# Kernel optimization log

Hardware: AMD Instinct MI355X
Metric: run time of the kernel (lower is better)

Reference implementation:

```python
import jax, jax.numpy as jnp
import numpy as np

B, T, E, H, D = 4, 2048, 1024, 16, 64


def setup_inputs() -> dict:
    key = jax.random.key(0)
    k1, k2, k3, k4 = jax.random.split(key, 4)
    s = 1.0 / np.sqrt(E)
    return {
        "x": jax.random.normal(k1, (B, T, E), dtype=jnp.float32),
        "wj_w": jax.random.uniform(k2, (E, E), jnp.float32, -s, s),   # torch Linear weight (out,in)
        "wjv_w": jax.random.uniform(k3, (E, E), jnp.float32, -s, s),
        "wo_w": jax.random.uniform(k4, (E, H * D), jnp.float32, -s, s),
    }


def reference(x, wj_w, wjv_w, wo_w):
    b, t, e = x.shape
    # echo = x @ wj_w.T ; eb = echo @ wj_w  (F.linear with transposed weight)
    eb = (x @ wj_w.T) @ wj_w
    sc = jnp.sum(x * eb, axis=-1) / jnp.sqrt(jnp.asarray(e, x.dtype))  # (B,T)
    # rank-1 outer-product scores with strict-upper causal mask
    ja = sc[:, :, None] * sc[:, None, :]                               # (B,T,T)
    causal = jnp.tril(jnp.ones((t, t), dtype=bool))
    ja = jnp.where(causal[None], ja, -jnp.inf)
    ja = jax.nn.softmax(ja, axis=-1)                                   # (B,T,T)
    # values per head; attention map shared across heads (broadcast, not materialized)
    val = (x @ wjv_w.T).reshape(b, t, H, D)                            # (B,T,H,D)
    out = jnp.einsum("bts,bshd->bthd", ja, val)                       # (B,T,H,D)
    return out.reshape(b, t, H * D) @ wo_w.T                           # (B,T,E)
```

## Files before the change

### kernel.cpp

```cpp
#include <hip/hip_runtime.h>
#include <math.h>

#define R_ROWS 8192
#define T_SEQ  2048
#define E_DIM  1024
#define KC     32
#define KCR    256
#define PBATCH_ELEMS ((size_t)4352 * 512)

typedef __attribute__((ext_vector_type(8))) short short8;
typedef __attribute__((ext_vector_type(4))) float f32x4;

__device__ __forceinline__ ushort f2bf(float f) {
  uint u = __float_as_uint(f);
  u += 0x7FFFu + ((u >> 16) & 1u);
  return (ushort)(u >> 16);
}
__device__ __forceinline__ float bf2f(ushort h) {
  return __uint_as_float(((uint)h) << 16);
}


__device__ __forceinline__ void split_frag_unit(
    const float* __restrict__ in, ushort* __restrict__ hi,
    ushort* __restrict__ lo, int g)
{
  const int l = g & 15, h = (g >> 4) & 3;
  const int pq = g >> 6;
  const int q = pq & (KC - 1), p = pq >> 5;
  const size_t src = (size_t)(p * 16 + l) * 1024 + q * 32 + h * 8;
  const float4 v0 = *(const float4*)&in[src];
  const float4 v1 = *(const float4*)&in[src + 4];
  ushort hh[8], ll[8];
  const float v[8] = {v0.x, v0.y, v0.z, v0.w, v1.x, v1.y, v1.z, v1.w};
#pragma unroll
  for (int e = 0; e < 8; ++e) {
    hh[e] = f2bf(v[e]);
    ll[e] = f2bf(v[e] - bf2f(hh[e]));
  }
  *(uint4*)&hi[(size_t)g * 8] = *(const uint4*)hh;
  *(uint4*)&lo[(size_t)g * 8] = *(const uint4*)ll;
}

__device__ __forceinline__ void splitT_frag_unit(
    const float* __restrict__ in, ushort* __restrict__ hi,
    ushort* __restrict__ lo, int g)
{
  const int l = g & 15, h = (g >> 4) & 3;
  const int pq = g >> 6;
  const int q = pq & (KC - 1), p = pq >> 5;
  const int rr = p * 16 + l;
  const int cc = q * 32 + h * 8;
  ushort hh[8], ll[8];
#pragma unroll
  for (int e = 0; e < 8; ++e) {
    const float v = in[(size_t)(cc + e) * 1024 + rr];
    hh[e] = f2bf(v);
    ll[e] = f2bf(v - bf2f(hh[e]));
  }
  *(uint4*)&hi[(size_t)g * 8] = *(const uint4*)hh;
  *(uint4*)&lo[(size_t)g * 8] = *(const uint4*)ll;
}

__global__ __launch_bounds__(256) void cvt_all(
    const float* __restrict__ x, const float* __restrict__ wo,
    const float* __restrict__ wjv, const float* __restrict__ wj,
    ushort* __restrict__ xh, ushort* __restrict__ xl,
    ushort* __restrict__ woh, ushort* __restrict__ wol,
    ushort* __restrict__ wjvh, ushort* __restrict__ wjvl,
    ushort* __restrict__ wjh, ushort* __restrict__ wjl,
    float* __restrict__ sc_raw, float* __restrict__ zsum)
{
  const int blk = blockIdx.x;
  const int tid = threadIdx.x;
  if (blk < 64) {
    const int idx = blk * 256 + tid;
    if (idx < R_ROWS) sc_raw[idx] = 0.f;
    else              zsum[idx - R_ROWS] = 0.f;
  }
  if (blk < 4096) {
    split_frag_unit(x, xh, xl, blk * 256 + tid);
  } else if (blk < 4608) {
    split_frag_unit(wo, woh, wol, (blk - 4096) * 256 + tid);
  } else if (blk < 5120) {
    splitT_frag_unit(wjv, wjvh, wjvl, (blk - 4608) * 256 + tid);
  } else {
    split_frag_unit(wj, wjh, wjl, (blk - 5120) * 256 + tid);
  }
}

struct Frags { short8 ah[4], al[4], bh[4], bl[4]; };

__global__ __launch_bounds__(256, 2) void gemm_sq_direct(
    const ushort* __restrict__ xh, const ushort* __restrict__ xl,
    const ushort* __restrict__ wh, const ushort* __restrict__ wl,
    float* __restrict__ sc_raw)
{
  const int tid = threadIdx.x;
  const int m0 = blockIdx.y * 128, n0 = blockIdx.x * 128;
  const int wave = tid >> 6, lane = tid & 63;
  const int l15 = lane & 15, lq = lane >> 4;
  const int wm = (wave & 1) * 64, wn = (wave >> 1) * 64;

  size_t aoff[4], boff[4];
#pragma unroll
  for (int i = 0; i < 4; ++i)
    aoff[i] = ((size_t)(((m0 + wm) >> 4) + i) * KC * 4 + lq) * 128 + l15 * 8;
#pragma unroll
  for (int j = 0; j < 4; ++j)
    boff[j] = ((size_t)(((n0 + wn) >> 4) + j) * KC * 4 + lq) * 128 + l15 * 8;

  f32x4 acc[4][4] = {};
  Frags f0, f1;

  auto load = [&](Frags& f, int q) {
    const size_t dq = (size_t)q * 512;
#pragma unroll
    for (int i = 0; i < 4; ++i) {
      f.ah[i] = *(const short8*)(xh + aoff[i] + dq);
      f.al[i] = *(const short8*)(xl + aoff[i] + dq);
    }
#pragma unroll
    for (int j = 0; j < 4; ++j) {
      f.bh[j] = *(const short8*)(wh + boff[j] + dq);
      f.bl[j] = *(const short8*)(wl + boff[j] + dq);
    }
  };
  auto step = [&](const Frags& f) {
#pragma unroll
    for (int i = 0; i < 4; ++i)
#pragma unroll
      for (int j = 0; j < 4; ++j) {
        acc[i][j] = __builtin_amdgcn_mfma_f32_16x16x32_bf16(f.ah[i], f.bh[j], acc[i][j], 0, 0, 0);
        acc[i][j] = __builtin_amdgcn_mfma_f32_16x16x32_bf16(f.ah[i], f.bl[j], acc[i][j], 0, 0, 0);
        acc[i][j] = __builtin_amdgcn_mfma_f32_16x16x32_bf16(f.al[i], f.bh[j], acc[i][j], 0, 0, 0);
      }
  };

  load(f0, 0);
#pragma unroll 1
  for (int q = 0; q < KC; q += 2) {
    load(f1, q + 1);
    step(f0);
    if (q + 2 < KC) load(f0, q + 2);
    step(f1);
  }

  __shared__ float red[128][33];
#pragma unroll
  for (int i = 0; i < 4; ++i)
#pragma unroll
    for (int r = 0; r < 4; ++r) {
      const int row = wm + i * 16 + lq * 4 + r;
      float s = 0.f;
#pragma unroll
      for (int j = 0; j < 4; ++j) s += acc[i][j][r] * acc[i][j][r];
      red[row][(l15 << 1) | (wave >> 1)] = s;
    }
  __syncthreads();
  if (tid < 128) {
    float s = 0.f;
#pragma unroll
    for (int c = 0; c < 32; ++c) s += red[tid][c];
    atomicAdd(&sc_raw[m0 + tid], s);
  }
}

struct Frags2 { short8 ah[2], al[2], bh[2], bl[2]; };

__global__ __launch_bounds__(256, 2) void gemm_m_split(
    const ushort* __restrict__ ah_, const ushort* __restrict__ al_,
    const ushort* __restrict__ bh_, const ushort* __restrict__ bl_,
    ushort* __restrict__ Mf)
{
  const int tid = threadIdx.x;
  const int m0 = blockIdx.y * 64, n0 = blockIdx.x * 64;
  const int wave = tid >> 6, lane = tid & 63;
  const int l15 = lane & 15, lq = lane >> 4;
  const int wm = (wave & 1) * 32, wn = (wave >> 1) * 32;

  size_t aoff[2], boff[2];
#pragma unroll
  for (int i = 0; i < 2; ++i)
    aoff[i] = ((size_t)(((m0 + wm) >> 4) + i) * KC * 4 + lq) * 128 + l15 * 8;
#pragma unroll
  for (int j = 0; j < 2; ++j)
    boff[j] = ((size_t)(((n0 + wn) >> 4) + j) * KC * 4 + lq) * 128 + l15 * 8;

  f32x4 acc[2][2] = {};
  Frags2 f0, f1;

  auto load = [&](Frags2& f, int q) {
    const size_t dq = (size_t)q * 512;
#pragma unroll
    for (int i = 0; i < 2; ++i) {
      f.ah[i] = *(const short8*)(ah_ + aoff[i] + dq);
      f.al[i] = *(const short8*)(al_ + aoff[i] + dq);
    }
#pragma unroll
    for (int j = 0; j < 2; ++j) {
      f.bh[j] = *(const short8*)(bh_ + boff[j] + dq);
      f.bl[j] = *(const short8*)(bl_ + boff[j] + dq);
    }
  };
  auto step = [&](const Frags2& f) {
#pragma unroll
    for (int i = 0; i < 2; ++i)
#pragma unroll
      for (int j = 0; j < 2; ++j) {
        acc[i][j] = __builtin_amdgcn_mfma_f32_16x16x32_bf16(f.ah[i], f.bh[j], acc[i][j], 0, 0, 0);
        acc[i][j] = __builtin_amdgcn_mfma_f32_16x16x32_bf16(f.ah[i], f.bl[j], acc[i][j], 0, 0, 0);
        acc[i][j] = __builtin_amdgcn_mfma_f32_16x16x32_bf16(f.al[i], f.bh[j], acc[i][j], 0, 0, 0);
      }
  };

  load(f0, 0);
#pragma unroll 1
  for (int q = 0; q < KC; q += 2) {
    load(f1, q + 1);
    step(f0);
    if (q + 2 < KC) load(f0, q + 2);
    step(f1);
  }

#pragma unroll
  for (int i = 0; i < 2; ++i)
#pragma unroll
    for (int j = 0; j < 2; ++j) {
      const int fb = m0 + wm + i * 16 + lq * 4;
      const int k  = n0 + wn + j * 16 + l15;
#pragma unroll
      for (int r = 0; r < 4; ++r) {
        const int f = fb + r;
        const size_t addr =
            (((size_t)(f >> 4) * KC + (k >> 5)) * 4 + ((k >> 3) & 3)) * 128 +
            (f & 15) * 8 + (k & 7);
        Mf[addr] = f2bf(acc[i][j][r]);
      }
    }
}

__global__ __launch_bounds__(512) void pgen2(
    const float* __restrict__ sc_raw, ushort* __restrict__ P012,
    ushort* __restrict__ P3, float* __restrict__ zsum)
{
  const int y = blockIdx.x, b = blockIdx.y, zslice = blockIdx.z;
  const int bT = b * T_SEQ;
  ushort* pb = (b < 3) ? P012 + (size_t)b * PBATCH_ELEMS : P3;
  __shared__ float scs[T_SEQ];
  __shared__ float pma[T_SEQ];
  __shared__ float pmb[T_SEQ];
  const int tid = threadIdx.x;
  for (int i = tid; i < T_SEQ; i += 512) {
    const float v = sc_raw[bT + i] * 0.03125f;
    scs[i] = v;
    pma[i] = v;
  }
  __syncthreads();
  float* src = pma; float* dst = pmb;
  for (int off = 1; off < T_SEQ; off <<= 1) {
    for (int i = tid; i < T_SEQ; i += 512)
      dst[i] = (i >= off) ? fmaxf(src[i], src[i - off]) : src[i];
    __syncthreads();
    float* t = src; src = dst; dst = t;
  }
  const float* pms = src;

  const int lane = tid & 63;
  const int hi = lane >> 4, l = lane & 15;

#pragma unroll 1
  for (int ph = 0; ph < 2; ++ph) {
    const int P = ph ? y : 15 - y;
    const int W = 4 * P + 4;
    ushort* base = pb + (size_t)(16 * P * (P + 1)) * 512;
    const int nu = 512 * W;
#pragma unroll 1
    for (int u = tid + zslice * 512; u < nu; u += 8192) {
      const int pr = (u >> 6) & 7, q = u >> 9;
      const int t = P * 128 + pr * 16 + l;
      const int s0 = q * 32 + hi * 8;
      const float st = scs[t], pm = pms[t];
      ushort tmp[8];
      float z = 0.f;
#pragma unroll
      for (int e = 0; e < 8; ++e) {
        const int s = s0 + e;
        float pe = 0.f;
        if (s <= t) pe = __expf(st * (scs[s] - pm));
        tmp[e] = f2bf(pe);
        z += pe;
      }
      *(uint4*)&base[(size_t)(pr * W + q) * 512 + hi * 128 + l * 8] =
          *(const uint4*)tmp;
      z += __shfl_xor(z, 16);
      z += __shfl_xor(z, 32);
      if (hi == 0) atomicAdd(&zsum[bT + t], z);
    }
  }
}

struct FP2 { short8 a[2][4]; short8 b[2][4]; };

__global__ __launch_bounds__(256, 2) void gemm_wt(
    const ushort* __restrict__ Af, const ushort* __restrict__ Bf,
    ushort* __restrict__ WT)
{
  const int tid = threadIdx.x;
  const int m0 = blockIdx.y * 128, n0 = blockIdx.x * 128;
  const int wave = tid >> 6, lane = tid & 63;
  const int l15 = lane & 15, lq = lane >> 4;
  const int wm = (wave & 1) * 64, wn = (wave >> 1) * 64;

  size_t aoff[4], boff[4];
#pragma unroll
  for (int i = 0; i < 4; ++i)
    aoff[i] = ((size_t)(((m0 + wm) >> 4) + i) * KC * 4 + lq) * 128 + l15 * 8;
#pragma unroll
  for (int j = 0; j < 4; ++j)
    boff[j] = ((size_t)(((n0 + wn) >> 4) + j) * KC * 4 + lq) * 128 + l15 * 8;

  f32x4 acc[4][4] = {};
  FP2 f0, f1;

  auto load2 = [&](FP2& f, int q) {
#pragma unroll
    for (int c = 0; c < 2; ++c) {
      const size_t dq = (size_t)(q + c) * 512;
#pragma unroll
      for (int i = 0; i < 4; ++i) f.a[c][i] = *(const short8*)(Af + aoff[i] + dq);
#pragma unroll
      for (int j = 0; j < 4; ++j) f.b[c][j] = *(const short8*)(Bf + boff[j] + dq);
    }
  };
  auto step2 = [&](const FP2& f) {
#pragma unroll
    for (int c = 0; c < 2; ++c)
#pragma unroll
      for (int i = 0; i < 4; ++i)
#pragma unroll
        for (int j = 0; j < 4; ++j)
          acc[i][j] = __builtin_amdgcn_mfma_f32_16x16x32_bf16(f.a[c][i], f.b[c][j], acc[i][j], 0, 0, 0);
  };

  load2(f0, 0);
#pragma unroll 1
  for (int q = 0; q < KC; q += 4) {
    load2(f1, q + 2);
    step2(f0);
    if (q + 4 < KC) load2(f0, q + 4);
    step2(f1);
  }

#pragma unroll
  for (int i = 0; i < 4; ++i)
#pragma unroll
    for (int j = 0; j < 4; ++j) {
      const int eb = m0 + wm + i * 16 + lq * 4;
      const int rg = n0 + wn + j * 16 + l15;
#pragma unroll
      for (int r = 0; r < 4; ++r) {
        const int e = eb + r;
        const size_t addr =
            (((size_t)(e >> 4) * KCR + (rg >> 5)) * 4 + ((rg >> 3) & 3)) * 128 +
            (e & 15) * 8 + (rg & 7);
        WT[addr] = f2bf(acc[i][j][r]);
      }
    }
}

struct FA2 { short8 a[2][4]; short8 b[2][2]; };

__global__ __launch_bounds__(512) void attn_gemm(
    const ushort* __restrict__ P012, const ushort* __restrict__ P3,
    const ushort* __restrict__ WT, const float* __restrict__ zsum,
    float* __restrict__ outp)
{
  const int b = blockIdx.z, y = blockIdx.y;
  const int e0 = blockIdx.x * 128;
  const int bT = b * T_SEQ;
  const ushort* pb = (b < 3) ? P012 + (size_t)b * PBATCH_ELEMS : P3;
  const int tid = threadIdx.x;
  const int wave = tid >> 6, lane = tid & 63;
  const int l15 = lane & 15, lq = lane >> 4;
  const int wm = (wave & 1) * 64;
  const int wn = (wave >> 1) * 32;

  size_t boff[2];
#pragma unroll
  for (int j = 0; j < 2; ++j)
    boff[j] = ((size_t)((((e0 + wn) >> 4) + j) * KCR + (bT >> 5)) * 4 + lq) * 128
              + l15 * 8;

#pragma unroll 1
  for (int ph = 0; ph < 2; ++ph) {
    const int ty = ph ? y : 15 - y;
    const int W = 4 * ty + 4;
    const int t0 = ty * 128;

    size_t aoff[4];
#pragma unroll
    for (int i = 0; i < 4; ++i)
      aoff[i] = ((size_t)(16 * ty * (ty + 1)) + (size_t)((wm >> 4) + i) * W) * 512
                + lq * 128 + l15 * 8;

    f32x4 acc[4][2] = {};
    FA2 f0, f1;

    auto load2 = [&](FA2& f, int q) {
#pragma unroll
      for (int c = 0; c < 2; ++c) {
        const size_t dq = (size_t)(q + c) * 512;
#pragma unroll
        for (int i = 0; i < 4; ++i) f.a[c][i] = *(const short8*)(pb + aoff[i] + dq);
#pragma unroll
        for (int j = 0; j < 2; ++j) f.b[c][j] = *(const short8*)(WT + boff[j] + dq);
      }
    };
    auto step2 = [&](const FA2& f) {
#pragma unroll
      for (int c = 0; c < 2; ++c)
#pragma unroll
        for (int i = 0; i < 4; ++i)
#pragma unroll
          for (int j = 0; j < 2; ++j)
            acc[i][j] = __builtin_amdgcn_mfma_f32_16x16x32_bf16(
                f.a[c][i], f.b[c][j], acc[i][j], 0, 0, 0);
    };

    load2(f0, 0);
#pragma unroll 1
    for (int q = 0; q < W; q += 4) {
      load2(f1, q + 2);
      step2(f0);
      if (q + 4 < W) load2(f0, q + 4);
      step2(f1);
    }

#pragma unroll
    for (int i = 0; i < 4; ++i)
#pragma unroll
      for (int r = 0; r < 4; ++r) {
        const int row = t0 + wm + i * 16 + lq * 4 + r;
        const float zi = 1.0f / zsum[bT + row];
#pragma unroll
        for (int j = 0; j < 2; ++j) {
          const int nb = e0 + wn + j * 16 + l15;
          outp[(size_t)(bT + row) * E_DIM + nb] = acc[i][j][r] * zi;
        }
      }
  }
}

extern "C" void kernel_launch(void* const* d_in, const int* in_sizes, int n_in,
                              void* d_out, int out_size, void* d_ws, size_t ws_size,
                              hipStream_t stream) {
  (void)in_sizes; (void)n_in; (void)out_size; (void)ws_size;
  const float* x   = (const float*)d_in[0];
  const float* wj  = (const float*)d_in[1];
  const float* wjv = (const float*)d_in[2];
  const float* wo  = (const float*)d_in[3];
  float* out = (float*)d_out;

  ushort* xh_f  = (ushort*)d_ws;
  ushort* xl_f  = xh_f  + (size_t)R_ROWS * E_DIM;
  ushort* woh   = xl_f  + (size_t)R_ROWS * E_DIM;
  ushort* wol   = woh   + (size_t)E_DIM * E_DIM;
  ushort* wjvh  = wol   + (size_t)E_DIM * E_DIM;
  ushort* wjvl  = wjvh  + (size_t)E_DIM * E_DIM;
  ushort* wjh   = wjvl  + (size_t)E_DIM * E_DIM;
  ushort* wjl   = wjh   + (size_t)E_DIM * E_DIM;
  ushort* Mf    = wjl   + (size_t)E_DIM * E_DIM;
  float* sc_raw = (float*)(Mf + (size_t)E_DIM * E_DIM);
  float* zsum   = sc_raw + R_ROWS;
  ushort* WT    = xl_f;
  ushort* P012  = xh_f;
  ushort* P3    = woh;

  cvt_all<<<5632, 256, 0, stream>>>(x, wo, wjv, wj,
                                    xh_f, xl_f, woh, wol, wjvh, wjvl, wjh, wjl,
                                    sc_raw, zsum);

  gemm_m_split<<<dim3(E_DIM/64, E_DIM/64), 256, 0, stream>>>(
      woh, wol, wjvh, wjvl, Mf);

  gemm_sq_direct<<<dim3(E_DIM/128, R_ROWS/128), 256, 0, stream>>>(
      xh_f, xl_f, wjh, wjl, sc_raw);

  gemm_wt<<<dim3(R_ROWS/128, E_DIM/128), 256, 0, stream>>>(Mf, xh_f, WT);

  pgen2<<<dim3(8, 4, 16), 512, 0, stream>>>(sc_raw, P012, P3, zsum);

  attn_gemm<<<dim3(E_DIM/128, 8, 4), 512, 0, stream>>>(P012, P3, WT, zsum, out);
}
```

Measured before the change: 263.8 us.

## Merge independent sq and M GEMMs into one launch, add sched barriers

Fuses the two independent GEMM kernels (squared-norm score GEMM and the wo·wjv M-matrix GEMM) into a single launch that dispatches on block index. This removes one kernel launch and lets the small M GEMM's blocks fill the GPU alongside the score GEMM's tail instead of running serially. It also inserts sched_barrier calls in the gemm_wt and attention GEMM main loops so the compiler keeps prefetch loads grouped ahead of the MFMA step. The barriers constrain instruction scheduling and may help or hurt latency hiding, and the merged kernel's register use is set by the larger branch.

```diff
diff --git a/kernel.cpp b/kernel.cpp
--- a/kernel.cpp
+++ b/kernel.cpp
@@ -90,154 +90,152 @@
 }
 
 struct Frags { short8 ah[4], al[4], bh[4], bl[4]; };
-
-__global__ __launch_bounds__(256, 2) void gemm_sq_direct(
+struct Frags2 { short8 ah[2], al[2], bh[2], bl[2]; };
+
+__global__ __launch_bounds__(256, 2) void gemm_sq_m(
     const ushort* __restrict__ xh, const ushort* __restrict__ xl,
     const ushort* __restrict__ wh, const ushort* __restrict__ wl,
-    float* __restrict__ sc_raw)
-{
-  const int tid = threadIdx.x;
-  const int m0 = blockIdx.y * 128, n0 = blockIdx.x * 128;
-  const int wave = tid >> 6, lane = tid & 63;
-  const int l15 = lane & 15, lq = lane >> 4;
-  const int wm = (wave & 1) * 64, wn = (wave >> 1) * 64;
-
-  size_t aoff[4], boff[4];
-#pragma unroll
-  for (int i = 0; i < 4; ++i)
-    aoff[i] = ((size_t)(((m0 + wm) >> 4) + i) * KC * 4 + lq) * 128 + l15 * 8;
-#pragma unroll
-  for (int j = 0; j < 4; ++j)
-    boff[j] = ((size_t)(((n0 + wn) >> 4) + j) * KC * 4 + lq) * 128 + l15 * 8;
-
-  f32x4 acc[4][4] = {};
-  Frags f0, f1;
-
-  auto load = [&](Frags& f, int q) {
-    const size_t dq = (size_t)q * 512;
-#pragma unroll
-    for (int i = 0; i < 4; ++i) {
-      f.ah[i] = *(const short8*)(xh + aoff[i] + dq);
-      f.al[i] = *(const short8*)(xl + aoff[i] + dq);
-    }
-#pragma unroll
-    for (int j = 0; j < 4; ++j) {
-      f.bh[j] = *(const short8*)(wh + boff[j] + dq);
-      f.bl[j] = *(const short8*)(wl + boff[j] + dq);
-    }
-  };
-  auto step = [&](const Frags& f) {
-#pragma unroll
-    for (int i = 0; i < 4; ++i)
-#pragma unroll
-      for (int j = 0; j < 4; ++j) {
-        acc[i][j] = __builtin_amdgcn_mfma_f32_16x16x32_bf16(f.ah[i], f.bh[j], acc[i][j], 0, 0, 0);
-        acc[i][j] = __builtin_amdgcn_mfma_f32_16x16x32_bf16(f.ah[i], f.bl[j], acc[i][j], 0, 0, 0);
-        acc[i][j] = __builtin_amdgcn_mfma_f32_16x16x32_bf16(f.al[i], f.bh[j], acc[i][j], 0, 0, 0);
-      }
-  };
-
-  load(f0, 0);
-#pragma unroll 1
-  for (int q = 0; q < KC; q += 2) {
-    load(f1, q + 1);
-    step(f0);
-    if (q + 2 < KC) load(f0, q + 2);
-    step(f1);
-  }
-
-  __shared__ float red[128][33];
-#pragma unroll
-  for (int i = 0; i < 4; ++i)
-#pragma unroll
-    for (int r = 0; r < 4; ++r) {
-      const int row = wm + i * 16 + lq * 4 + r;
-      float s = 0.f;
-#pragma unroll
-      for (int j = 0; j < 4; ++j) s += acc[i][j][r] * acc[i][j][r];
-      red[row][(l15 << 1) | (wave >> 1)] = s;
-    }
-  __syncthreads();
-  if (tid < 128) {
-    float s = 0.f;
-#pragma unroll
-    for (int c = 0; c < 32; ++c) s += red[tid][c];
-    atomicAdd(&sc_raw[m0 + tid], s);
-  }
-}
-
-struct Frags2 { short8 ah[2], al[2], bh[2], bl[2]; };
-
-__global__ __launch_bounds__(256, 2) void gemm_m_split(
+    float* __restrict__ sc_raw,
     const ushort* __restrict__ ah_, const ushort* __restrict__ al_,
     const ushort* __restrict__ bh_, const ushort* __restrict__ bl_,
     ushort* __restrict__ Mf)
 {
+  const int blk = blockIdx.x;
   const int tid = threadIdx.x;
-  const int m0 = blockIdx.y * 64, n0 = blockIdx.x * 64;
   const int wave = tid >> 6, lane = tid & 63;
   const int l15 = lane & 15, lq = lane >> 4;
-  const int wm = (wave & 1) * 32, wn = (wave >> 1) * 32;
-
-  size_t aoff[2], boff[2];
-#pragma unroll
-  for (int i = 0; i < 2; ++i)
-    aoff[i] = ((size_t)(((m0 + wm) >> 4) + i) * KC * 4 + lq) * 128 + l15 * 8;
-#pragma unroll
-  for (int j = 0; j < 2; ++j)
-    boff[j] = ((size_t)(((n0 + wn) >> 4) + j) * KC * 4 + lq) * 128 + l15 * 8;
-
-  f32x4 acc[2][2] = {};
-  Frags2 f0, f1;
-
-  auto load = [&](Frags2& f, int q) {
-    const size_t dq = (size_t)q * 512;
-#pragma unroll
-    for (int i = 0; i < 2; ++i) {
-      f.ah[i] = *(const short8*)(ah_ + aoff[i] + dq);
-      f.al[i] = *(const short8*)(al_ + aoff[i] + dq);
-    }
-#pragma unroll
-    for (int j = 0; j < 2; ++j) {
-      f.bh[j] = *(const short8*)(bh_ + boff[j] + dq);
-      f.bl[j] = *(const short8*)(bl_ + boff[j] + dq);
-    }
-  };
-  auto step = [&](const Frags2& f) {
+
+  if (blk < 512) {
+    const int m0 = (blk >> 3) * 128, n0 = (blk & 7) * 128;
+    const int wm = (wave & 1) * 64, wn = (wave >> 1) * 64;
+
+    size_t aoff[4], boff[4];
+#pragma unroll
+    for (int i = 0; i < 4; ++i)
+      aoff[i] = ((size_t)(((m0 + wm) >> 4) + i) * KC * 4 + lq) * 128 + l15 * 8;
+#pragma unroll
+    for (int j = 0; j < 4; ++j)
+      boff[j] = ((size_t)(((n0 + wn) >> 4) + j) * KC * 4 + lq) * 128 + l15 * 8;
+
+    f32x4 acc[4][4] = {};
+    Frags f0, f1;
+
+    auto load = [&](Frags& f, int q) {
+      const size_t dq = (size_t)q * 512;
+#pragma unroll
+      for (int i = 0; i < 4; ++i) {
+        f.ah[i] = *(const short8*)(xh + aoff[i] + dq);
+        f.al[i] = *(const short8*)(xl + aoff[i] + dq);
+      }
+#pragma unroll
+      for (int j = 0; j < 4; ++j) {
+        f.bh[j] = *(const short8*)(wh + boff[j] + dq);
+        f.bl[j] = *(const short8*)(wl + boff[j] + dq);
+      }
+    };
+    auto step = [&](const Frags& f) {
+#pragma unroll
+      for (int i = 0; i < 4; ++i)
+#pragma unroll
+        for (int j = 0; j < 4; ++j) {
+          acc[i][j] = __builtin_amdgcn_mfma_f32_16x16x32_bf16(f.ah[i], f.bh[j], acc[i][j], 0, 0, 0);
+          acc[i][j] = __builtin_amdgcn_mfma_f32_16x16x32_bf16(f.ah[i], f.bl[j], acc[i][j], 0, 0, 0);
+          acc[i][j] = __builtin_amdgcn_mfma_f32_16x16x32_bf16(f.al[i], f.bh[j], acc[i][j], 0, 0, 0);
+        }
+    };
+
+    load(f0, 0);
+#pragma unroll 1
+    for (int q = 0; q < KC; q += 2) {
+      load(f1, q + 1);
+      step(f0);
+      if (q + 2 < KC) load(f0, q + 2);
+      step(f1);
+    }
+
+    __shared__ float red[128][33];
+#pragma unroll
+    for (int i = 0; i < 4; ++i)
+#pragma unroll
+      for (int r = 0; r < 4; ++r) {
+        const int row = wm + i * 16 + lq * 4 + r;
+        float s = 0.f;
+#pragma unroll
+        for (int j = 0; j < 4; ++j) s += acc[i][j][r] * acc[i][j][r];
+        red[row][(l15 << 1) | (wave >> 1)] = s;
+      }
+    __syncthreads();
+    if (tid < 128) {
+      float s = 0.f;
+#pragma unroll
+      for (int c = 0; c < 32; ++c) s += red[tid][c];
+      atomicAdd(&sc_raw[m0 + tid], s);
+    }
+  } else {
+    const int mm = blk - 512;
+    const int m0 = (mm >> 4) * 64, n0 = (mm & 15) * 64;
+    const int wm = (wave & 1) * 32, wn = (wave >> 1) * 32;
+
+    size_t aoff[2], boff[2];
 #pragma unroll
     for (int i = 0; i < 2; ++i)
+      aoff[i] = ((size_t)(((m0 + wm) >> 4) + i) * KC * 4 + lq) * 128 + l15 * 8;
+#pragma unroll
+    for (int j = 0; j < 2; ++j)
+      boff[j] = ((size_t)(((n0 + wn) >> 4) + j) * KC * 4 + lq) * 128 + l15 * 8;
+
+    f32x4 acc[2][2] = {};
+    Frags2 f0, f1;
+
+    auto load = [&](Frags2& f, int q) {
+      const size_t dq = (size_t)q * 512;
+#pragma unroll
+      for (int i = 0; i < 2; ++i) {
+        f.ah[i] = *(const short8*)(ah_ + aoff[i] + dq);
+        f.al[i] = *(const short8*)(al_ + aoff[i] + dq);
+      }
 #pragma unroll
       for (int j = 0; j < 2; ++j) {
-        acc[i][j] = __builtin_amdgcn_mfma_f32_16x16x32_bf16(f.ah[i], f.bh[j], acc[i][j], 0, 0, 0);
-        acc[i][j] = __builtin_amdgcn_mfma_f32_16x16x32_bf16(f.ah[i], f.bl[j], acc[i][j], 0, 0, 0);
-        acc[i][j] = __builtin_amdgcn_mfma_f32_16x16x32_bf16(f.al[i], f.bh[j], acc[i][j], 0, 0, 0);
-      }
-  };
-
-  load(f0, 0);
-#pragma unroll 1
-  for (int q = 0; q < KC; q += 2) {
-    load(f1, q + 1);
-    step(f0);
-    if (q + 2 < KC) load(f0, q + 2);
-    step(f1);
-  }
-
-#pragma unroll
-  for (int i = 0; i < 2; ++i)
-#pragma unroll
-    for (int j = 0; j < 2; ++j) {
-      const int fb = m0 + wm + i * 16 + lq * 4;
-      const int k  = n0 + wn + j * 16 + l15;
-#pragma unroll
-      for (int r = 0; r < 4; ++r) {
-        const int f = fb + r;
-        const size_t addr =
-            (((size_t)(f >> 4) * KC + (k >> 5)) * 4 + ((k >> 3) & 3)) * 128 +
-            (f & 15) * 8 + (k & 7);
-        Mf[addr] = f2bf(acc[i][j][r]);
-      }
-    }
+        f.bh[j] = *(const short8*)(bh_ + boff[j] + dq);
+        f.bl[j] = *(const short8*)(bl_ + boff[j] + dq);
+      }
+    };
+    auto step = [&](const Frags2& f) {
+#pragma unroll
+      for (int i = 0; i < 2; ++i)
+#pragma unroll
+        for (int j = 0; j < 2; ++j) {
+          acc[i][j] = __builtin_amdgcn_mfma_f32_16x16x32_bf16(f.ah[i], f.bh[j], acc[i][j], 0, 0, 0);
+          acc[i][j] = __builtin_amdgcn_mfma_f32_16x16x32_bf16(f.ah[i], f.bl[j], acc[i][j], 0, 0, 0);
+          acc[i][j] = __builtin_amdgcn_mfma_f32_16x16x32_bf16(f.al[i], f.bh[j], acc[i][j], 0, 0, 0);
+        }
+    };
+
+    load(f0, 0);
+#pragma unroll 1
+    for (int q = 0; q < KC; q += 2) {
+      load(f1, q + 1);
+      step(f0);
+      if (q + 2 < KC) load(f0, q + 2);
+      step(f1);
+    }
+
+#pragma unroll
+    for (int i = 0; i < 2; ++i)
+#pragma unroll
+      for (int j = 0; j < 2; ++j) {
+        const int fb = m0 + wm + i * 16 + lq * 4;
+        const int k  = n0 + wn + j * 16 + l15;
+#pragma unroll
+        for (int r = 0; r < 4; ++r) {
+          const int f = fb + r;
+          const size_t addr =
+              (((size_t)(f >> 4) * KC + (k >> 5)) * 4 + ((k >> 3) & 3)) * 128 +
+              (f & 15) * 8 + (k & 7);
+          Mf[addr] = f2bf(acc[i][j][r]);
+        }
+      }
+  }
 }
 
 __global__ __launch_bounds__(512) void pgen2(
@@ -344,11 +342,16 @@
   };
 
   load2(f0, 0);
+  __builtin_amdgcn_sched_barrier(0);
 #pragma unroll 1
   for (int q = 0; q < KC; q += 4) {
     load2(f1, q + 2);
+    __builtin_amdgcn_sched_barrier(0);
     step2(f0);
-    if (q + 4 < KC) load2(f0, q + 4);
+    if (q + 4 < KC) {
+      load2(f0, q + 4);
+      __builtin_amdgcn_sched_barrier(0);
+    }
     step2(f1);
   }
 
@@ -429,11 +432,16 @@
     };
 
     load2(f0, 0);
+    __builtin_amdgcn_sched_barrier(0);
 #pragma unroll 1
     for (int q = 0; q < W; q += 4) {
       load2(f1, q + 2);
+      __builtin_amdgcn_sched_barrier(0);
       step2(f0);
-      if (q + 4 < W) load2(f0, q + 4);
+      if (q + 4 < W) {
+        load2(f0, q + 4);
+        __builtin_amdgcn_sched_barrier(0);
+      }
       step2(f1);
     }
 
@@ -481,11 +489,8 @@
                                     xh_f, xl_f, woh, wol, wjvh, wjvl, wjh, wjl,
                                     sc_raw, zsum);
 
-  gemm_m_split<<<dim3(E_DIM/64, E_DIM/64), 256, 0, stream>>>(
-      woh, wol, wjvh, wjvl, Mf);
-
-  gemm_sq_direct<<<dim3(E_DIM/128, R_ROWS/128), 256, 0, stream>>>(
-      xh_f, xl_f, wjh, wjl, sc_raw);
+  gemm_sq_m<<<768, 256, 0, stream>>>(xh_f, xl_f, wjh, wjl, sc_raw,
+                                     woh, wol, wjvh, wjvl, Mf);
 
   gemm_wt<<<dim3(R_ROWS/128, E_DIM/128), 256, 0, stream>>>(Mf, xh_f, WT);
 
```

Result: faster. 243.8 us (-7.6%).
